# Kernel tuning notes

Measured on AMD Instinct MI355X. Metric: run time of the kernel, lower is better.

Reference implementation:

```python
import jax, jax.numpy as jnp
import numpy as np

VOCAB = 1000
MAX_T = 1000  # max_episode_length
L = 64        # instruction length


def _uniform(key, shape, fan_in, fan_out):
    bound = float(np.sqrt(6.0 / (fan_in + fan_out)))
    return jax.random.uniform(key, shape, jnp.float32, -bound, bound)


def setup_inputs() -> dict:
    key = jax.random.key(0)
    ks = jax.random.split(key, 20)
    s = float(1.0 / np.sqrt(256.0))
    inp = {}
    inp['x'] = jax.random.normal(ks[0], (1, 400), jnp.float32)
    inp['input_inst'] = jax.random.randint(ks[1], (1, L), 0, VOCAB)
    inp['tx'] = jax.random.randint(ks[2], (1,), 0, MAX_T + 1)
    inp['hx'] = jax.random.normal(ks[3], (1, 256), jnp.float32) * 0.1
    inp['cx'] = jax.random.normal(ks[4], (1, 256), jnp.float32) * 0.1
    inp['img1_w'] = _uniform(ks[5], (128, 400), 400, 128); inp['img1_b'] = jnp.zeros((128,), jnp.float32)
    inp['img2_w'] = _uniform(ks[6], (128, 128), 128, 128); inp['img2_b'] = jnp.zeros((128,), jnp.float32)
    inp['img3_w'] = _uniform(ks[7], (128, 128), 128, 128); inp['img3_b'] = jnp.zeros((128,), jnp.float32)
    inp['emb'] = jax.random.normal(ks[8], (VOCAB, 32), jnp.float32)
    inp['gru_wi'] = jax.random.uniform(ks[9], (768, 32), jnp.float32, -s, s)
    inp['gru_wh'] = jax.random.uniform(ks[10], (768, 256), jnp.float32, -s, s)
    inp['gru_bi'] = jnp.zeros((768,), jnp.float32); inp['gru_bh'] = jnp.zeros((768,), jnp.float32)
    inp['attn_w'] = _uniform(ks[11], (128, 256), 256, 128); inp['attn_b'] = jnp.zeros((128,), jnp.float32)
    inp['time_emb'] = jax.random.normal(ks[12], (MAX_T + 1, 32), jnp.float32)
    inp['lin_w'] = _uniform(ks[13], (256, 128), 128, 256); inp['lin_b'] = jnp.zeros((256,), jnp.float32)
    inp['lstm_wi'] = jax.random.uniform(ks[14], (1024, 256), jnp.float32, -s, s)
    inp['lstm_wh'] = jax.random.uniform(ks[15], (1024, 256), jnp.float32, -s, s)
    inp['lstm_bi'] = jnp.zeros((1024,), jnp.float32); inp['lstm_bh'] = jnp.zeros((1024,), jnp.float32)
    inp['crit_w'] = jax.random.normal(ks[16], (1, 288), jnp.float32) * 0.06
    inp['crit_b'] = jnp.zeros((1,), jnp.float32)
    inp['act_w'] = jax.random.normal(ks[17], (4, 288), jnp.float32) * 0.01
    inp['act_b'] = jnp.zeros((4,), jnp.float32)
    return inp


def _linear(x, w, b):
    return x @ w.T + b


def reference(x, input_inst, tx, hx, cx,
              img1_w, img1_b, img2_w, img2_b, img3_w, img3_b,
              emb, gru_wi, gru_wh, gru_bi, gru_bh,
              attn_w, attn_b, time_emb, lin_w, lin_b,
              lstm_wi, lstm_wh, lstm_bi, lstm_bh,
              crit_w, crit_b, act_w, act_b):
    # image MLP: 400 -> 128 -> 128 -> 128
    h = jax.nn.relu(_linear(x.reshape(x.shape[0], -1), img1_w, img1_b))
    h = jax.nn.relu(_linear(h, img2_w, img2_b))
    x_image_rep = jax.nn.relu(_linear(h, img3_w, img3_b))  # (1,128)

    # GRU encoder over instruction tokens (torch gate order: r, z, n)
    emb_seq = emb[input_inst[0]]  # (L, 32)

    def gru_step(hg, e):
        gi = gru_wi @ e + gru_bi        # (768,)
        gh = gru_wh @ hg + gru_bh       # (768,)
        ir, iz, i_n = jnp.split(gi, 3)
        hr, hz, hn = jnp.split(gh, 3)
        r = jax.nn.sigmoid(ir + hr)
        z = jax.nn.sigmoid(iz + hz)
        n = jnp.tanh(i_n + r * hn)
        return (1.0 - z) * n + z * hg, None

    h_enc, _ = jax.lax.scan(gru_step, jnp.zeros((256,), x.dtype), emb_seq)
    x_instr_rep = h_enc[None, :]  # (1,256)

    # gated attention fusion
    x_attention = jax.nn.sigmoid(_linear(x_instr_rep, attn_w, attn_b))  # (1,128)
    fused = x_image_rep * x_attention
    fused = jax.nn.relu(_linear(fused, lin_w, lin_b))  # (1,256)

    # LSTMCell (torch gate order: i, f, g, o)
    gates = fused @ lstm_wi.T + lstm_bi + hx @ lstm_wh.T + lstm_bh  # (1,1024)
    i_g, f_g, g_g, o_g = jnp.split(gates, 4, axis=1)
    c_new = jax.nn.sigmoid(f_g) * cx + jax.nn.sigmoid(i_g) * jnp.tanh(g_g)
    h_new = jax.nn.sigmoid(o_g) * jnp.tanh(c_new)

    t_emb = time_emb[tx].reshape(-1, 32)  # (1,32)
    feat = jnp.concatenate([h_new, t_emb], axis=1)  # (1,288)
    return _linear(feat, crit_w, crit_b), _linear(feat, act_w, act_b), h_new, c_new
```

## Files before the change

### kernel.cpp

```cpp
#include <hip/hip_runtime.h>
#include <math.h>


typedef __fp16 h2 __attribute__((ext_vector_type(2)));
typedef __fp16 h8 __attribute__((ext_vector_type(8)));

#define WS_IMG    0
#define WS_GATESH 128
#define WS_FUSED  1152
#define WS_GI     1408
#define WS_REGW   50560
#define WS_LDSW   124288

__device__ __forceinline__ float dot4(const float4 a, const float4 b){
  return a.x*b.x + a.y*b.y + a.z*b.z + a.w*b.w;
}
__device__ __forceinline__ float sigm(float x){ return 1.f/(1.f+expf(-x)); }

#define P0(v) __builtin_shufflevector(v,v,0,1)
#define P1(v) __builtin_shufflevector(v,v,2,3)
#define P2(v) __builtin_shufflevector(v,v,4,5)
#define P3(v) __builtin_shufflevector(v,v,6,7)
#define PK(a,b) __builtin_amdgcn_cvt_pkrtz(a,b)
#define FD(w,e,acc) __builtin_amdgcn_fdot2(w,e,acc,false)

__global__ __launch_bounds__(256) void a3c_pre(
    const float* __restrict__ x,
    const float* __restrict__ i1w, const float* __restrict__ i1b,
    const float* __restrict__ i2w, const float* __restrict__ i2b,
    const float* __restrict__ i3w, const float* __restrict__ i3b,
    const float* __restrict__ hx,  const float* __restrict__ lwh,
    const float* __restrict__ lbh,
    const int*   __restrict__ tx,  const float* __restrict__ temb,
    const float* __restrict__ cw,  const float* __restrict__ cb,
    const float* __restrict__ acw, const float* __restrict__ acb,
    const int*   __restrict__ inst, const float* __restrict__ emb,
    const float* __restrict__ gwi,  const float* __restrict__ gbi,
    const float* __restrict__ gwh,
    float* __restrict__ ws, float* __restrict__ out)
{
  const int b = blockIdx.x;
  const int t = threadIdx.x;

  if (b == 0) {
    __shared__ __align__(16) float x_lds[400];
    __shared__ __align__(16) float h1[128];
    __shared__ __align__(16) float h2s[128];
    x_lds[t] = x[t];
    if (t < 144) x_lds[256+t] = x[256+t];
    __syncthreads();
    {
      const int o = t>>1, half = t&1;
      const float4* wr = (const float4*)(i1w + o*400 + half*200);
      const float4* xr = (const float4*)(x_lds + half*200);
      float acc = 0.f;
      #pragma unroll 5
      for (int k=0;k<50;++k) acc += dot4(wr[k], xr[k]);
      acc += __shfl_down(acc, 1, 2);
      if (half == 0) h1[o] = fmaxf(acc + i1b[o], 0.f);
    }
    __syncthreads();
    if (t < 128){
      const float4* wr = (const float4*)(i2w + t*128);
      const float4* h4 = (const float4*)h1;
      float acc = i2b[t];
      #pragma unroll 8
      for (int k=0;k<32;++k) acc += dot4(wr[k], h4[k]);
      h2s[t] = fmaxf(acc, 0.f);
    }
    __syncthreads();
    if (t < 128){
      const float4* wr = (const float4*)(i3w + t*128);
      const float4* h4 = (const float4*)h2s;
      float acc = i3b[t];
      #pragma unroll 8
      for (int k=0;k<32;++k) acc += dot4(wr[k], h4[k]);
      ws[WS_IMG + t] = fmaxf(acc, 0.f);
    }

  } else if (b <= 4) {
    __shared__ __align__(16) float hx_lds[256];
    hx_lds[t] = hx[t];
    __syncthreads();
    const int R = (b-1)*256 + t;
    const float4* wr = (const float4*)(lwh + R*256);
    const float4* h4 = (const float4*)hx_lds;
    float acc = lbh[R];
    #pragma unroll 8
    for (int k=0;k<64;++k) acc += dot4(wr[k], h4[k]);
    ws[WS_GATESH + R] = acc;

  } else if (b == 5) {
    if (t < 64){
      float tv = 0.f;
      if (t < 32) tv = temb[tx[0]*32 + t];
      #pragma unroll
      for (int o=0;o<5;++o){
        const float* wrow = (o==0) ? cw : (acw + (o-1)*288);
        float pr = (t < 32) ? tv*wrow[256+t] : 0.f;
        #pragma unroll
        for (int off=16; off; off>>=1) pr += __shfl_down(pr, off, 32);
        if (t == 0) out[o] = pr + ((o==0) ? cb[0] : acb[o-1]);
      }
    }

  } else if (b < 198) {
    const int idx = (b-6)*256 + t;
    const int s = idx / 768;
    const int r = idx - s*768;
    const float4* wr = (const float4*)(gwi + r*32);
    const float4* er = (const float4*)(emb + inst[s]*32);
    float acc = gbi[r];
    #pragma unroll
    for (int k=0;k<8;++k) acc += dot4(wr[k], er[k]);
    ws[WS_GI + idx] = acc;

  } else if (b < 486) {
    const int d = (b-198)*256 + t;
    const int e = d*2;
    const int tt  = e / 144;  int rem = e - tt*144;
    const int rho = rem / 48; rem -= rho*48;
    const int k   = rem >> 3;
    const int el  = rem & 7;
    const int q = tt >> 2, i = tt & 3;
    const int row = 3*q + rho;
    const int col = 64 + ((k<<2)+i)*8 + el;
    ((h2*)(ws + WS_REGW))[d] = PK(gwh[row*256+col], gwh[row*256+col+1]);

  } else {
    const int d = (b-486)*256 + t;
    const int e = d*2;
    const int row = e / 72;
    const int col = e - row*72;
    float a0 = 0.f, a1 = 0.f;
    if (col < 64){ a0 = gwh[row*256+col]; a1 = gwh[row*256+col+1]; }
    ((h2*)(ws + WS_LDSW))[d] = PK(a0, a1);
  }
}

__global__ __attribute__((amdgpu_flat_work_group_size(1024,1024),
                          amdgpu_waves_per_eu(4,4)))
void a3c_scan(
    const float* __restrict__ gbh,
    const float* __restrict__ aw,  const float* __restrict__ ab,
    const float* __restrict__ lnw, const float* __restrict__ lnb,
    float* __restrict__ ws)
{
  const int t = threadIdx.x;
  const int q = t >> 2, i = t & 3;
  const int r0 = 3*q, r1 = 3*q+1, r2 = 3*q+2;

  __shared__ __align__(16) __fp16 lw_[768*72];
  __shared__ __align__(16) __fp16 h16[256];
  __shared__ float h32[256];
  __shared__ float pre[768];
  __shared__ float bhl[768];
  __shared__ float gil[2][768];
  __shared__ __align__(16) float f0[128];

  {
    const float4* src = (const float4*)(ws + WS_LDSW);
    float4* dst = (float4*)lw_;
    for (int n=t; n<6912; n+=1024) dst[n] = src[n];
  }
  if (t < 768){ bhl[t] = gbh[t]; gil[0][t] = ws[WS_GI + t]; }
  if (t < 256){ h16[t] = (__fp16)0.f; h32[t] = 0.f; }

  const h8* rw = (const h8*)(ws + WS_REGW) + t*18;
  const h8 W00=rw[0],  W01=rw[1],  W02=rw[2],  W03=rw[3],  W04=rw[4],  W05=rw[5];
  const h8 W10=rw[6],  W11=rw[7],  W12=rw[8],  W13=rw[9],  W14=rw[10], W15=rw[11];
  const h8 W20=rw[12], W21=rw[13], W22=rw[14], W23=rw[15], W24=rw[16], W25=rw[17];
  __syncthreads();

  int cur = 0;
  for (int s=0; s<64; ++s){
    float gnx = 0.f;
    if (t < 768) gnx = ws[WS_GI + ((s<63)?(s+1):63)*768 + t];

    float p0=0.f, p1=0.f, p2=0.f;
    {
      const h8 hva = *(const h8*)(h16 + (i<<3));
      const h8 hvb = *(const h8*)(h16 + ((i+4)<<3));
      #define LBLK(RR, PA) { \
        const h8 wa = *(const h8*)(lw_ + (RR)*72 + (i<<3)); \
        const h8 wb = *(const h8*)(lw_ + (RR)*72 + ((i+4)<<3)); \
        PA=FD(P0(wa),P0(hva),PA); PA=FD(P1(wa),P1(hva),PA); \
        PA=FD(P2(wa),P2(hva),PA); PA=FD(P3(wa),P3(hva),PA); \
        PA=FD(P0(wb),P0(hvb),PA); PA=FD(P1(wb),P1(hvb),PA); \
        PA=FD(P2(wb),P2(hvb),PA); PA=FD(P3(wb),P3(hvb),PA); }
      LBLK(r0,p0) LBLK(r1,p1) LBLK(r2,p2)
      #undef LBLK
    }
    #define RBLK(K) { \
      const h8 hv = *(const h8*)(h16 + ((8+((K)<<2)+i)<<3)); \
      p0=FD(P0(W0##K),P0(hv),p0); p0=FD(P1(W0##K),P1(hv),p0); \
      p0=FD(P2(W0##K),P2(hv),p0); p0=FD(P3(W0##K),P3(hv),p0); \
      p1=FD(P0(W1##K),P0(hv),p1); p1=FD(P1(W1##K),P1(hv),p1); \
      p1=FD(P2(W1##K),P2(hv),p1); p1=FD(P3(W1##K),P3(hv),p1); \
      p2=FD(P0(W2##K),P0(hv),p2); p2=FD(P1(W2##K),P1(hv),p2); \
      p2=FD(P2(W2##K),P2(hv),p2); p2=FD(P3(W2##K),P3(hv),p2); }
    RBLK(0) RBLK(1) RBLK(2) RBLK(3) RBLK(4) RBLK(5)
    #undef RBLK

    p0 += __shfl_xor(p0,1); p0 += __shfl_xor(p0,2);
    p1 += __shfl_xor(p1,1); p1 += __shfl_xor(p1,2);
    p2 += __shfl_xor(p2,1); p2 += __shfl_xor(p2,2);
    if (i < 3){
      const int row = 3*q + i;
      const float pv = (i==0) ? p0 : ((i==1) ? p1 : p2);
      pre[row] = pv + bhl[row];
    }
    if (t < 768) gil[cur^1][t] = gnx;
    __syncthreads();
    if (t < 256){
      const float rr = sigm(gil[cur][t]       + pre[t]);
      const float zz = sigm(gil[cur][256 + t] + pre[256 + t]);
      const float nn = tanhf(gil[cur][512 + t] + rr*pre[512 + t]);
      const float hv = (1.f - zz)*nn + zz*h32[t];
      h32[t] = hv;
      h16[t] = (__fp16)hv;
    }
    cur ^= 1;
    __syncthreads();
  }

  if (t < 128){
    const float4* wr = (const float4*)(aw + t*256);
    const float4* h4 = (const float4*)h32;
    float acc = ab[t];
    #pragma unroll 8
    for (int k=0;k<64;++k) acc += dot4(wr[k], h4[k]);
    f0[t] = ws[WS_IMG + t] * sigm(acc);
  }
  __syncthreads();
  if (t < 256){
    const float4* wr = (const float4*)(lnw + t*128);
    const float4* h4 = (const float4*)f0;
    float acc = lnb[t];
    #pragma unroll 8
    for (int k=0;k<32;++k) acc += dot4(wr[k], h4[k]);
    ws[WS_FUSED + t] = fmaxf(acc, 0.f);
  }
}

__global__ __launch_bounds__(256) void a3c_post(
    const float* __restrict__ lwi, const float* __restrict__ lbi,
    const float* __restrict__ cx,
    const float* __restrict__ cw,  const float* __restrict__ acw,
    float* __restrict__ ws, float* __restrict__ out)
{
  const int p = blockIdx.x;
  const int t = threadIdx.x;
  __shared__ __align__(16) float fused_lds[256];
  __shared__ float gv[256];
  __shared__ float hh[64];
  fused_lds[t] = ws[WS_FUSED + t];
  __syncthreads();
  const int g = t>>6, ul = t&63;
  const int R = (g<<8) + p*64 + ul;
  const float4* wr = (const float4*)(lwi + R*256);
  const float4* f4 = (const float4*)fused_lds;
  float acc = ws[WS_GATESH + R] + lbi[R];
  #pragma unroll 8
  for (int k=0;k<64;++k) acc += dot4(wr[k], f4[k]);
  gv[t] = acc;
  __syncthreads();
  if (t < 64){
    const int u2 = p*64 + t;
    const float iv = gv[t], fv = gv[64+t], gg = gv[128+t], ov = gv[192+t];
    const float c = sigm(fv)*cx[u2] + sigm(iv)*tanhf(gg);
    const float h = sigm(ov)*tanhf(c);
    out[5   + u2] = h;
    out[261 + u2] = c;
    hh[t] = h;
  }
  __syncthreads();
  if (t < 64){
    #pragma unroll
    for (int o=0;o<5;++o){
      const float* wrow = (o==0) ? cw : (acw + (o-1)*288);
      float pr = hh[t]*wrow[p*64 + t];
      #pragma unroll
      for (int off=32; off; off>>=1) pr += __shfl_down(pr, off, 64);
      if (t == 0) atomicAdd(out + o, pr);
    }
  }
}

extern "C" void kernel_launch(void* const* d_in, const int* in_sizes, int n_in,
                              void* d_out, int out_size, void* d_ws, size_t ws_size,
                              hipStream_t stream) {
  (void)in_sizes; (void)n_in; (void)out_size; (void)ws_size;
  const float* x    = (const float*)d_in[0];
  const int*   inst = (const int*)  d_in[1];
  const int*   tx   = (const int*)  d_in[2];
  const float* hx   = (const float*)d_in[3];
  const float* cx   = (const float*)d_in[4];
  const float* i1w  = (const float*)d_in[5];
  const float* i1b  = (const float*)d_in[6];
  const float* i2w  = (const float*)d_in[7];
  const float* i2b  = (const float*)d_in[8];
  const float* i3w  = (const float*)d_in[9];
  const float* i3b  = (const float*)d_in[10];
  const float* emb  = (const float*)d_in[11];
  const float* gwi  = (const float*)d_in[12];
  const float* gwh  = (const float*)d_in[13];
  const float* gbi  = (const float*)d_in[14];
  const float* gbh  = (const float*)d_in[15];
  const float* aw   = (const float*)d_in[16];
  const float* ab   = (const float*)d_in[17];
  const float* temb = (const float*)d_in[18];
  const float* lnw  = (const float*)d_in[19];
  const float* lnb  = (const float*)d_in[20];
  const float* lwi  = (const float*)d_in[21];
  const float* lwh  = (const float*)d_in[22];
  const float* lbi  = (const float*)d_in[23];
  const float* lbh  = (const float*)d_in[24];
  const float* cw   = (const float*)d_in[25];
  const float* cb   = (const float*)d_in[26];
  const float* acw  = (const float*)d_in[27];
  const float* acb  = (const float*)d_in[28];
  float* ws  = (float*)d_ws;
  float* out = (float*)d_out;

  a3c_pre <<<594, 256, 0, stream>>>(x, i1w, i1b, i2w, i2b, i3w, i3b,
                                    hx, lwh, lbh, tx, temb, cw, cb, acw, acb,
                                    inst, emb, gwi, gbi, gwh, ws, out);
  a3c_scan<<<1, 1024, 0, stream>>>(gbh, aw, ab, lnw, lnb, ws);
  a3c_post<<<4, 256, 0, stream>>>(lwi, lbi, cx, cw, acw, ws, out);
}
```

Before: 143.9 us.

## Hold full GRU hidden weights in registers and reduce partials via LDS

The GRU recurrent matrix is now kept entirely in registers. Each thread holds 6 rows × 32 columns in fp16, pinned with asm so the compiler keeps them in VGPRs. The previous hybrid of LDS-resident weights plus register weights is dropped, along with the LDS staging copy and the corresponding pre-pass blocks. The 8-way partial sums are written to a padded LDS array and summed by the gate threads, replacing the shuffle reduction. This removes per-step LDS weight reads but raises register pressure and adds LDS traffic for the partials.

```diff
diff --git a/kernel.cpp b/kernel.cpp
--- a/kernel.cpp
+++ b/kernel.cpp
@@ -4,13 +4,13 @@
 
 typedef __fp16 h2 __attribute__((ext_vector_type(2)));
 typedef __fp16 h8 __attribute__((ext_vector_type(8)));
+typedef float  f4 __attribute__((ext_vector_type(4)));
 
 #define WS_IMG    0
 #define WS_GATESH 128
 #define WS_FUSED  1152
 #define WS_GI     1408
 #define WS_REGW   50560
-#define WS_LDSW   124288
 
 __device__ __forceinline__ float dot4(const float4 a, const float4 b){
   return a.x*b.x + a.y*b.y + a.z*b.z + a.w*b.w;
@@ -115,31 +115,21 @@
     for (int k=0;k<8;++k) acc += dot4(wr[k], er[k]);
     ws[WS_GI + idx] = acc;
 
-  } else if (b < 486) {
+  } else {
     const int d = (b-198)*256 + t;
-    const int e = d*2;
-    const int tt  = e / 144;  int rem = e - tt*144;
-    const int rho = rem / 48; rem -= rho*48;
-    const int k   = rem >> 3;
-    const int el  = rem & 7;
-    const int q = tt >> 2, i = tt & 3;
-    const int row = 3*q + rho;
-    const int col = 64 + ((k<<2)+i)*8 + el;
+    const int e = d << 1;
+    const int tt = e / 192;
+    int rem = e - tt*192;
+    const int rho = rem >> 5; rem &= 31;
+    const int c = rem >> 3;
+    const int el = rem & 7;
+    const int row = 6*(tt>>3) + rho;
+    const int col = ((tt&7)<<5) + (c<<3) + el;
     ((h2*)(ws + WS_REGW))[d] = PK(gwh[row*256+col], gwh[row*256+col+1]);
-
-  } else {
-    const int d = (b-486)*256 + t;
-    const int e = d*2;
-    const int row = e / 72;
-    const int col = e - row*72;
-    float a0 = 0.f, a1 = 0.f;
-    if (col < 64){ a0 = gwh[row*256+col]; a1 = gwh[row*256+col+1]; }
-    ((h2*)(ws + WS_LDSW))[d] = PK(a0, a1);
-  }
-}
-
-__global__ __attribute__((amdgpu_flat_work_group_size(1024,1024),
-                          amdgpu_waves_per_eu(4,4)))
+  }
+}
+
+__global__ __attribute__((amdgpu_flat_work_group_size(1024,1024)))
 void a3c_scan(
     const float* __restrict__ gbh,
     const float* __restrict__ aw,  const float* __restrict__ ab,
@@ -147,75 +137,76 @@
     float* __restrict__ ws)
 {
   const int t = threadIdx.x;
-  const int q = t >> 2, i = t & 3;
-  const int r0 = 3*q, r1 = 3*q+1, r2 = 3*q+2;
-
-  __shared__ __align__(16) __fp16 lw_[768*72];
+  const int o = t >> 3, i = t & 7;
+
   __shared__ __align__(16) __fp16 h16[256];
   __shared__ float h32[256];
-  __shared__ float pre[768];
+  __shared__ float pp[768*9];
   __shared__ float bhl[768];
   __shared__ float gil[2][768];
   __shared__ __align__(16) float f0[128];
 
-  {
-    const float4* src = (const float4*)(ws + WS_LDSW);
-    float4* dst = (float4*)lw_;
-    for (int n=t; n<6912; n+=1024) dst[n] = src[n];
-  }
   if (t < 768){ bhl[t] = gbh[t]; gil[0][t] = ws[WS_GI + t]; }
   if (t < 256){ h16[t] = (__fp16)0.f; h32[t] = 0.f; }
 
-  const h8* rw = (const h8*)(ws + WS_REGW) + t*18;
-  const h8 W00=rw[0],  W01=rw[1],  W02=rw[2],  W03=rw[3],  W04=rw[4],  W05=rw[5];
-  const h8 W10=rw[6],  W11=rw[7],  W12=rw[8],  W13=rw[9],  W14=rw[10], W15=rw[11];
-  const h8 W20=rw[12], W21=rw[13], W22=rw[14], W23=rw[15], W24=rw[16], W25=rw[17];
-  __syncthreads();
-
+  const f4* rw = (const f4*)(ws + WS_REGW) + t*24;
+  f4 W00=rw[0],  W01=rw[1],  W02=rw[2],  W03=rw[3];
+  f4 W10=rw[4],  W11=rw[5],  W12=rw[6],  W13=rw[7];
+  f4 W20=rw[8],  W21=rw[9],  W22=rw[10], W23=rw[11];
+  f4 W30=rw[12], W31=rw[13], W32=rw[14], W33=rw[15];
+  f4 W40=rw[16], W41=rw[17], W42=rw[18], W43=rw[19];
+  f4 W50=rw[20], W51=rw[21], W52=rw[22], W53=rw[23];
+  #define PIN(v) asm volatile("" : "+v"(v))
+  PIN(W00);PIN(W01);PIN(W02);PIN(W03);PIN(W10);PIN(W11);PIN(W12);PIN(W13);
+  PIN(W20);PIN(W21);PIN(W22);PIN(W23);PIN(W30);PIN(W31);PIN(W32);PIN(W33);
+  PIN(W40);PIN(W41);PIN(W42);PIN(W43);PIN(W50);PIN(W51);PIN(W52);PIN(W53);
+  #undef PIN
+  __syncthreads();
+
+  const int pbase = o*6;
   int cur = 0;
   for (int s=0; s<64; ++s){
     float gnx = 0.f;
-    if (t < 768) gnx = ws[WS_GI + ((s<63)?(s+1):63)*768 + t];
-
-    float p0=0.f, p1=0.f, p2=0.f;
-    {
-      const h8 hva = *(const h8*)(h16 + (i<<3));
-      const h8 hvb = *(const h8*)(h16 + ((i+4)<<3));
-      #define LBLK(RR, PA) { \
-        const h8 wa = *(const h8*)(lw_ + (RR)*72 + (i<<3)); \
-        const h8 wb = *(const h8*)(lw_ + (RR)*72 + ((i+4)<<3)); \
-        PA=FD(P0(wa),P0(hva),PA); PA=FD(P1(wa),P1(hva),PA); \
-        PA=FD(P2(wa),P2(hva),PA); PA=FD(P3(wa),P3(hva),PA); \
-        PA=FD(P0(wb),P0(hvb),PA); PA=FD(P1(wb),P1(hvb),PA); \
-        PA=FD(P2(wb),P2(hvb),PA); PA=FD(P3(wb),P3(hvb),PA); }
-      LBLK(r0,p0) LBLK(r1,p1) LBLK(r2,p2)
-      #undef LBLK
-    }
-    #define RBLK(K) { \
-      const h8 hv = *(const h8*)(h16 + ((8+((K)<<2)+i)<<3)); \
-      p0=FD(P0(W0##K),P0(hv),p0); p0=FD(P1(W0##K),P1(hv),p0); \
-      p0=FD(P2(W0##K),P2(hv),p0); p0=FD(P3(W0##K),P3(hv),p0); \
-      p1=FD(P0(W1##K),P0(hv),p1); p1=FD(P1(W1##K),P1(hv),p1); \
-      p1=FD(P2(W1##K),P2(hv),p1); p1=FD(P3(W1##K),P3(hv),p1); \
-      p2=FD(P0(W2##K),P0(hv),p2); p2=FD(P1(W2##K),P1(hv),p2); \
-      p2=FD(P2(W2##K),P2(hv),p2); p2=FD(P3(W2##K),P3(hv),p2); }
-    RBLK(0) RBLK(1) RBLK(2) RBLK(3) RBLK(4) RBLK(5)
-    #undef RBLK
-
-    p0 += __shfl_xor(p0,1); p0 += __shfl_xor(p0,2);
-    p1 += __shfl_xor(p1,1); p1 += __shfl_xor(p1,2);
-    p2 += __shfl_xor(p2,1); p2 += __shfl_xor(p2,2);
-    if (i < 3){
-      const int row = 3*q + i;
-      const float pv = (i==0) ? p0 : ((i==1) ? p1 : p2);
-      pre[row] = pv + bhl[row];
-    }
+    if (t < 768) gnx = ws[WS_GI + ((s<63)?(s+1):s)*768 + t];
+
+    float a0=0.f,a1=0.f,a2=0.f,a3=0.f,a4=0.f,a5=0.f;
+    #define CHUNK(c) { \
+      const h8 hv = *(const h8*)(h16 + (i<<5) + ((c)<<3)); h8 w; \
+      w=__builtin_bit_cast(h8,W0##c); \
+      a0=FD(P0(w),P0(hv),a0); a0=FD(P1(w),P1(hv),a0); \
+      a0=FD(P2(w),P2(hv),a0); a0=FD(P3(w),P3(hv),a0); \
+      w=__builtin_bit_cast(h8,W1##c); \
+      a1=FD(P0(w),P0(hv),a1); a1=FD(P1(w),P1(hv),a1); \
+      a1=FD(P2(w),P2(hv),a1); a1=FD(P3(w),P3(hv),a1); \
+      w=__builtin_bit_cast(h8,W2##c); \
+      a2=FD(P0(w),P0(hv),a2); a2=FD(P1(w),P1(hv),a2); \
+      a2=FD(P2(w),P2(hv),a2); a2=FD(P3(w),P3(hv),a2); \
+      w=__builtin_bit_cast(h8,W3##c); \
+      a3=FD(P0(w),P0(hv),a3); a3=FD(P1(w),P1(hv),a3); \
+      a3=FD(P2(w),P2(hv),a3); a3=FD(P3(w),P3(hv),a3); \
+      w=__builtin_bit_cast(h8,W4##c); \
+      a4=FD(P0(w),P0(hv),a4); a4=FD(P1(w),P1(hv),a4); \
+      a4=FD(P2(w),P2(hv),a4); a4=FD(P3(w),P3(hv),a4); \
+      w=__builtin_bit_cast(h8,W5##c); \
+      a5=FD(P0(w),P0(hv),a5); a5=FD(P1(w),P1(hv),a5); \
+      a5=FD(P2(w),P2(hv),a5); a5=FD(P3(w),P3(hv),a5); }
+    CHUNK(0) CHUNK(1) CHUNK(2) CHUNK(3)
+    #undef CHUNK
+
+    pp[(pbase+0)*9+i]=a0; pp[(pbase+1)*9+i]=a1; pp[(pbase+2)*9+i]=a2;
+    pp[(pbase+3)*9+i]=a3; pp[(pbase+4)*9+i]=a4; pp[(pbase+5)*9+i]=a5;
     if (t < 768) gil[cur^1][t] = gnx;
     __syncthreads();
     if (t < 256){
-      const float rr = sigm(gil[cur][t]       + pre[t]);
-      const float zz = sigm(gil[cur][256 + t] + pre[256 + t]);
-      const float nn = tanhf(gil[cur][512 + t] + rr*pre[512 + t]);
+      const float* pr = pp + t*9;
+      const float* pz = pp + (256+t)*9;
+      const float* pn = pp + (512+t)*9;
+      float sr=bhl[t], sz=bhl[256+t], sn=bhl[512+t];
+      #pragma unroll
+      for (int k=0;k<8;++k){ sr+=pr[k]; sz+=pz[k]; sn+=pn[k]; }
+      const float rr = sigm(gil[cur][t]       + sr);
+      const float zz = sigm(gil[cur][256 + t] + sz);
+      const float nn = tanhf(gil[cur][512 + t] + rr*sn);
       const float hv = (1.f - zz)*nn + zz*h32[t];
       h32[t] = hv;
       h16[t] = (__fp16)hv;
@@ -259,10 +250,10 @@
   const int g = t>>6, ul = t&63;
   const int R = (g<<8) + p*64 + ul;
   const float4* wr = (const float4*)(lwi + R*256);
-  const float4* f4 = (const float4*)fused_lds;
+  const float4* f4p = (const float4*)fused_lds;
   float acc = ws[WS_GATESH + R] + lbi[R];
   #pragma unroll 8
-  for (int k=0;k<64;++k) acc += dot4(wr[k], f4[k]);
+  for (int k=0;k<64;++k) acc += dot4(wr[k], f4p[k]);
   gv[t] = acc;
   __syncthreads();
   if (t < 64){
@@ -323,7 +314,7 @@
   float* ws  = (float*)d_ws;
   float* out = (float*)d_out;
 
-  a3c_pre <<<594, 256, 0, stream>>>(x, i1w, i1b, i2w, i2b, i3w, i3b,
+  a3c_pre <<<582, 256, 0, stream>>>(x, i1w, i1b, i2w, i2b, i3w, i3b,
                                     hx, lwh, lbh, tx, temb, cw, cb, acw, acb,
                                     inst, emb, gwi, gbi, gwh, ws, out);
   a3c_scan<<<1, 1024, 0, stream>>>(gbh, aw, ab, lnw, lnb, ws);
```

Result: faster. 125.8 us (median of 2 runs) (-12.6%).
